# Kernel optimization log

Hardware: AMD Instinct MI355X
Metric: run time of the kernel (lower is better)

The kernel has to match this reference:

```python
import jax, jax.numpy as jnp
import numpy as np

GAMMA = 2.0                  # n2n_gamma
WAVELET_WEIGHT = 0.05
THRESHOLD = 50.0 / 255.0     # wavelet_threshold normalized
LEVELS = 3


def conv_model(x, weight):
    # Stand-in denoising network: 1->1 channel 3x3 SAME conv.
    return jax.lax.conv_general_dilated(
        x, weight, window_strides=(1, 1), padding='SAME',
        dimension_numbers=('NCHW', 'OIHW', 'NCHW'))


def generate_subimages_checkerboard(noisy):
    # 2x2 checkerboard: (even,even) and (odd,odd), bilinearly upsampled back
    # to (H, W). jax.image.resize 'linear' uses half-pixel centers, matching
    # torch F.interpolate(mode='bilinear', align_corners=False).
    B, C, H, W = noisy.shape  # H, W assumed even (512)
    p0 = noisy[:, :, 0::2, 0::2]
    p3 = noisy[:, :, 1::2, 1::2]
    g1 = jax.image.resize(p0, (B, C, H, W), method='linear')
    g2 = jax.image.resize(p3, (B, C, H, W), method='linear')
    return g1, g2


def haar_level(x):
    # One level of batched 2D Haar DWT on x: [B, H, W] (H, W even).
    a = x[:, 0::2, 0::2]
    b = x[:, 0::2, 1::2]
    c = x[:, 1::2, 0::2]
    d = x[:, 1::2, 1::2]
    ll = (a + b + c + d) * 0.5
    lh = (a - b + c - d) * 0.5  # horizontal detail
    hl = (a + b - c - d) * 0.5  # vertical detail
    hh = (a - b - c + d) * 0.5  # diagonal detail
    return ll, (lh, hl, hh)


def wavelet_sparsity_loss(pred):
    # pred: [B, C, H, W]; only channel 0 is used (as in the original).
    # L1(c, soft_threshold(c, t)) == mean(min(|c|, t)) since the target is
    # detached; pywt's coeffs[1] is the COARSEST detail level, with
    # threshold t/2^(level_idx-1) and weight 1/level_idx, so the finest
    # decomposition step j maps to level_idx = LEVELS - j + 1.
    x = pred[:, 0]  # [B, H, W]
    total = jnp.asarray(0.0, dtype=x.dtype)
    cur = x
    for j in range(1, LEVELS + 1):  # j=1 finest
        cur, (h, v, d) = haar_level(cur)
        level_idx = LEVELS - j + 1
        thr = THRESHOLD / (2.0 ** (level_idx - 1))
        w = 1.0 / level_idx
        lvl = (jnp.mean(jnp.minimum(jnp.abs(h), thr)) +
               jnp.mean(jnp.minimum(jnp.abs(v), thr)) +
               jnp.mean(jnp.minimum(jnp.abs(d), thr))) / 3.0
        total = total + w * lvl
    return total


def setup_inputs() -> dict:
    key = jax.random.key(0)
    k1, k2 = jax.random.split(key)
    noisy_input = jax.random.uniform(k1, (32, 1, 512, 512), dtype=jnp.float32)
    weight = jax.random.normal(k2, (1, 1, 3, 3), dtype=jnp.float32) * (1.0 / 3.0)
    return {"noisy_input": noisy_input, "weight": weight}


def reference(noisy_input, weight):
    g1, g2 = generate_subimages_checkerboard(noisy_input)
    out = jnp.clip(conv_model(g1, weight), 0.0, 1.0)
    rec = jnp.mean((out - g2) ** 2)
    reg = jnp.mean((out - g1) ** 2)
    n2n_total = rec + GAMMA * reg
    # Original detaches pred to numpy for the wavelet prior -> no gradient.
    wavelet = jax.lax.stop_gradient(wavelet_sparsity_loss(out))
    return n2n_total + WAVELET_WEIGHT * wavelet
```

## Files before the change

kernel.cpp:

```cpp
#include <hip/hip_runtime.h>

namespace {

constexpr int IMG = 512;
constexpr int S = 8;
constexpr int NSTRIPS = IMG / S;
constexpr int NWAVES = 32 * NSTRIPS;
constexpr int NBLK = NWAVES / 4;
constexpr float THR = 50.0f / 255.0f;

constexpr double N_PIX = 32.0 * 512.0 * 512.0;
constexpr double N_L1  = 32.0 * 256.0 * 256.0;
constexpr double N_L2  = 32.0 * 128.0 * 128.0;
constexpr double N_L3  = 32.0 * 64.0 * 64.0;
constexpr double C_REC = 1.0 / N_PIX;
constexpr double C_REG = 2.0 / N_PIX;
constexpr double C_W1  = 0.05 / (9.0 * N_L1);
constexpr double C_W2  = 0.05 / (6.0 * N_L2);
constexpr double C_W3  = 0.05 / (3.0 * N_L3);

struct F4 { float v[4]; };
struct F8 { float v[8]; };
struct Row { F8 g; float gl, gr; };

__device__ __forceinline__ F8 hblend(const F4& p, int lane) {
  float left  = __shfl_up(p.v[3], 1);
  float right = __shfl_down(p.v[0], 1);
  if (lane == 0)  left  = p.v[0];
  if (lane == 63) right = p.v[3];
  F8 h;
  h.v[0] = 0.25f*left   + 0.75f*p.v[0];
  h.v[1] = 0.75f*p.v[0] + 0.25f*p.v[1];
  h.v[2] = 0.25f*p.v[0] + 0.75f*p.v[1];
  h.v[3] = 0.75f*p.v[1] + 0.25f*p.v[2];
  h.v[4] = 0.25f*p.v[1] + 0.75f*p.v[2];
  h.v[5] = 0.75f*p.v[2] + 0.25f*p.v[3];
  h.v[6] = 0.25f*p.v[2] + 0.75f*p.v[3];
  h.v[7] = 0.75f*p.v[3] + 0.25f*right;
  return h;
}

__device__ __forceinline__ Row vblend(const F8& a, const F8& b, float wa, float wb, int lane) {
  Row r;
#pragma unroll
  for (int c = 0; c < 8; ++c) r.g.v[c] = wa*a.v[c] + wb*b.v[c];
  const float gl = __shfl_up(r.g.v[7], 1);
  const float gr = __shfl_down(r.g.v[0], 1);
  r.gl = (lane == 0)  ? 0.0f : gl;
  r.gr = (lane == 63) ? 0.0f : gr;
  return r;
}

__device__ __forceinline__ void conv_acc(const Row& r, const float* wk3, F8& acc) {
#pragma unroll
  for (int c = 0; c < 8; ++c) {
    const float gm1 = (c == 0) ? r.gl : r.g.v[c-1];
    const float gp1 = (c == 7) ? r.gr : r.g.v[c+1];
    acc.v[c] += wk3[0]*gm1 + wk3[1]*r.g.v[c] + wk3[2]*gp1;
  }
}

__device__ __forceinline__ F8 conv3(const Row& r0, const Row& r1, const Row& r2,
                                    const float* wk) {
  F8 o;
#pragma unroll
  for (int c = 0; c < 8; ++c) o.v[c] = 0.0f;
  conv_acc(r0, wk + 0, o);
  conv_acc(r1, wk + 3, o);
  conv_acc(r2, wk + 6, o);
#pragma unroll
  for (int c = 0; c < 8; ++c) o.v[c] = fminf(fmaxf(o.v[c], 0.0f), 1.0f);
  return o;
}

__device__ __forceinline__ F4 haarL1(const F8& e, const F8& o, float thr, float& acc) {
  F4 ll;
#pragma unroll
  for (int c = 0; c < 4; ++c) {
    const float a = e.v[2*c], b = e.v[2*c+1], cc = o.v[2*c], d = o.v[2*c+1];
    ll.v[c] = (a + b + cc + d) * 0.5f;
    const float lh = (a - b + cc - d) * 0.5f;
    const float hl = (a + b - cc - d) * 0.5f;
    const float hh = (a - b - cc + d) * 0.5f;
    acc += fminf(fabsf(lh), thr) + fminf(fabsf(hl), thr) + fminf(fabsf(hh), thr);
  }
  return ll;
}

__device__ __forceinline__ float haar1pair(float a, float b, float cc, float d,
                                           float thr, float& acc) {
  const float lh = (a - b + cc - d) * 0.5f;
  const float hl = (a + b - cc - d) * 0.5f;
  const float hh = (a - b - cc + d) * 0.5f;
  acc += fminf(fabsf(lh), thr) + fminf(fabsf(hl), thr) + fminf(fabsf(hh), thr);
  return (a + b + cc + d) * 0.5f;
}

__global__ __launch_bounds__(256, 2) void n2n_wavelet_kernel(
    const float* __restrict__ noisy,
    const float* __restrict__ weight,
    double* __restrict__ partial) {
  const int t = threadIdx.x;
  const int lane = t & 63;
  const int gwid = blockIdx.x * 4 + (t >> 6);
  const int strip = gwid & (NSTRIPS - 1);
  const int b = gwid >> 6;
  const float* base = noisy + (size_t)b * IMG * IMG + lane * 8;

  const int y0 = strip * S;
  const int k0 = y0 >> 1;
  const bool lastStrip = (y0 == IMG - S);

  float4 le0[6], le1[6], lo0[6], lo1[6];
#pragma unroll
  for (int i = 0; i < 6; ++i) {
    int r = k0 - 1 + i;
    r = r < 0 ? 0 : (r > 255 ? 255 : r);
    const float* pe = base + (2 * r) * IMG;
    const float* po = base + (2 * r + 1) * IMG;
    le0[i] = *(const float4*)pe;
    le1[i] = *(const float4*)(pe + 4);
    lo0[i] = *(const float4*)po;
    lo1[i] = *(const float4*)(po + 4);
  }

  float wk[9];
#pragma unroll
  for (int i = 0; i < 9; ++i) wk[i] = weight[i];

  F8 h0[6], h3[6];
#pragma unroll
  for (int i = 0; i < 6; ++i) {
    F4 e, o;
    e.v[0] = le0[i].x; e.v[1] = le0[i].z; e.v[2] = le1[i].x; e.v[3] = le1[i].z;
    o.v[0] = lo0[i].y; o.v[1] = lo0[i].w; o.v[2] = lo1[i].y; o.v[3] = lo1[i].w;
    h0[i] = hblend(e, lane);
    h3[i] = hblend(o, lane);
  }

  float rec = 0.f, rgg = 0.f, w1a = 0.f, w2a = 0.f, w3a = 0.f;
  const float thr1 = THR * 0.25f, thr2 = THR * 0.5f;

  Row g1m, g1c;
  if (y0 == 0) {
#pragma unroll
    for (int c = 0; c < 8; ++c) g1m.g.v[c] = 0.f;
    g1m.gl = 0.f; g1m.gr = 0.f;
  } else {
    g1m = vblend(h0[0], h0[1], 0.75f, 0.25f, lane);
  }
  g1c = vblend(h0[0], h0[1], 0.25f, 0.75f, lane);

  F4 ll1Prev;
  float ll2Prev0 = 0.f, ll2Prev1 = 0.f;

#pragma unroll
  for (int p = 0; p < 4; ++p) {
    const Row g1p = vblend(h0[p + 1], h0[p + 2], 0.75f, 0.25f, lane);

    const F8 outE = conv3(g1m, g1c, g1p, wk);
#pragma unroll
    for (int c = 0; c < 8; ++c) {
      const float g2 = 0.25f * h3[p].v[c] + 0.75f * h3[p + 1].v[c];
      float d = outE.v[c] - g2;        rec += d*d;
      d = outE.v[c] - g1c.g.v[c];      rgg += d*d;
    }

    Row g1q = vblend(h0[p + 1], h0[p + 2], 0.25f, 0.75f, lane);
    if (lastStrip && p == 3) {
#pragma unroll
      for (int c = 0; c < 8; ++c) g1q.g.v[c] = 0.f;
      g1q.gl = 0.f; g1q.gr = 0.f;
    }

    const F8 outO = conv3(g1c, g1p, g1q, wk);
#pragma unroll
    for (int c = 0; c < 8; ++c) {
      const float g2 = 0.75f * h3[p + 1].v[c] + 0.25f * h3[p + 2].v[c];
      float d = outO.v[c] - g2;        rec += d*d;
      d = outO.v[c] - g1p.g.v[c];      rgg += d*d;
    }

    const F4 ll1 = haarL1(outE, outO, thr1, w1a);
    if ((p & 1) == 0) {
      ll1Prev = ll1;
    } else {
      const float ll20 = haar1pair(ll1Prev.v[0], ll1Prev.v[1], ll1.v[0], ll1.v[1], thr2, w2a);
      const float ll21 = haar1pair(ll1Prev.v[2], ll1Prev.v[3], ll1.v[2], ll1.v[3], thr2, w2a);
      if (p == 1) {
        ll2Prev0 = ll20; ll2Prev1 = ll21;
      } else {
        const float lh = (ll2Prev0 - ll2Prev1 + ll20 - ll21) * 0.5f;
        const float hl = (ll2Prev0 + ll2Prev1 - ll20 - ll21) * 0.5f;
        const float hh = (ll2Prev0 - ll2Prev1 - ll20 + ll21) * 0.5f;
        w3a += fminf(fabsf(lh), THR) + fminf(fabsf(hl), THR) + fminf(fabsf(hh), THR);
      }
    }

    g1m = g1p; g1c = g1q;
  }

  float vals[5] = {rec, rgg, w1a, w2a, w3a};
#pragma unroll
  for (int v = 0; v < 5; ++v) {
#pragma unroll
    for (int off = 32; off > 0; off >>= 1) vals[v] += __shfl_down(vals[v], off);
  }
  if (lane == 0) {
    partial[gwid] = C_REC*(double)vals[0] + C_REG*(double)vals[1]
                  + C_W1*(double)vals[2] + C_W2*(double)vals[3] + C_W3*(double)vals[4];
  }
}

__global__ __launch_bounds__(256) void finalize_kernel(
    const double* __restrict__ partial, float* __restrict__ out) {
  __shared__ double sRed[4];
  const int t = threadIdx.x;
  double s = 0.0;
#pragma unroll
  for (int i = 0; i < NWAVES / 256; ++i) s += partial[i * 256 + t];
#pragma unroll
  for (int off = 32; off > 0; off >>= 1) s += __shfl_down(s, off);
  if ((t & 63) == 0) sRed[t >> 6] = s;
  __syncthreads();
  if (t == 0) out[0] = (float)(sRed[0] + sRed[1] + sRed[2] + sRed[3]);
}

}

extern "C" void kernel_launch(void* const* d_in, const int* in_sizes, int n_in,
                              void* d_out, int out_size, void* d_ws, size_t ws_size,
                              hipStream_t stream) {
  const float* noisy  = (const float*)d_in[0];
  const float* weight = (const float*)d_in[1];
  double* partial = (double*)d_ws;
  float* out = (float*)d_out;

  hipLaunchKernelGGL(n2n_wavelet_kernel, dim3(NBLK), dim3(256), 0, stream,
                     noisy, weight, partial);
  hipLaunchKernelGGL(finalize_kernel, dim3(1), dim3(256), 0, stream, partial, out);
}
```

Baseline: 84.39 us.

## Halve strip height and pair waves via shared memory for level-3 Haar

Each wave now handles 4 output rows instead of 8, and blocks shrink to two waves, which doubles the number of waves and cuts per-wave register use. Because a level-3 Haar coefficient spans 8 rows, the two waves in a block exchange level-2 LL values through shared memory with a barrier. The weights are also made wave-uniform with readfirstlane. The intent is more occupancy and latency hiding, at the cost of more redundant halo row loads and blending per output row, plus a block-level sync.

Measured after the change: 89.11 us. 5.6% more time.

```diff
diff --git a/kernel.cpp b/kernel.cpp
--- a/kernel.cpp
+++ b/kernel.cpp
@@ -3,10 +3,10 @@
 namespace {
 
 constexpr int IMG = 512;
-constexpr int S = 8;
+constexpr int S = 4;
 constexpr int NSTRIPS = IMG / S;
 constexpr int NWAVES = 32 * NSTRIPS;
-constexpr int NBLK = NWAVES / 4;
+constexpr int NBLK = NWAVES / 2;
 constexpr float THR = 50.0f / 255.0f;
 
 constexpr double N_PIX = 32.0 * 512.0 * 512.0;
@@ -96,44 +96,42 @@
   return (a + b + cc + d) * 0.5f;
 }
 
-__global__ __launch_bounds__(256, 2) void n2n_wavelet_kernel(
+__global__ __launch_bounds__(128, 3) void n2n_wavelet_kernel(
     const float* __restrict__ noisy,
     const float* __restrict__ weight,
     double* __restrict__ partial) {
+  __shared__ float ll2sh[128];
   const int t = threadIdx.x;
   const int lane = t & 63;
-  const int gwid = blockIdx.x * 4 + (t >> 6);
+  const int widx = t >> 6;
+  const int gwid = blockIdx.x * 2 + widx;
   const int strip = gwid & (NSTRIPS - 1);
-  const int b = gwid >> 6;
+  const int b = gwid >> 7;
   const float* base = noisy + (size_t)b * IMG * IMG + lane * 8;
 
   const int y0 = strip * S;
   const int k0 = y0 >> 1;
-  const bool lastStrip = (y0 == IMG - S);
-
-  float4 le0[6], le1[6], lo0[6], lo1[6];
-#pragma unroll
-  for (int i = 0; i < 6; ++i) {
+  const bool lastStrip = (strip == NSTRIPS - 1);
+
+  float wk[9];
+#pragma unroll
+  for (int i = 0; i < 9; ++i)
+    wk[i] = __uint_as_float(__builtin_amdgcn_readfirstlane(__float_as_uint(weight[i])));
+
+  F8 h0[4], h3[4];
+#pragma unroll
+  for (int i = 0; i < 4; ++i) {
     int r = k0 - 1 + i;
     r = r < 0 ? 0 : (r > 255 ? 255 : r);
-    const float* pe = base + (2 * r) * IMG;
-    const float* po = base + (2 * r + 1) * IMG;
-    le0[i] = *(const float4*)pe;
-    le1[i] = *(const float4*)(pe + 4);
-    lo0[i] = *(const float4*)po;
-    lo1[i] = *(const float4*)(po + 4);
-  }
-
-  float wk[9];
-#pragma unroll
-  for (int i = 0; i < 9; ++i) wk[i] = weight[i];
-
-  F8 h0[6], h3[6];
-#pragma unroll
-  for (int i = 0; i < 6; ++i) {
+    const float* pe = base + (size_t)(2 * r) * IMG;
+    const float* po = pe + IMG;
+    const float4 e0 = *(const float4*)pe;
+    const float4 e1 = *(const float4*)(pe + 4);
+    const float4 o0 = *(const float4*)po;
+    const float4 o1 = *(const float4*)(po + 4);
     F4 e, o;
-    e.v[0] = le0[i].x; e.v[1] = le0[i].z; e.v[2] = le1[i].x; e.v[3] = le1[i].z;
-    o.v[0] = lo0[i].y; o.v[1] = lo0[i].w; o.v[2] = lo1[i].y; o.v[3] = lo1[i].w;
+    e.v[0] = e0.x; e.v[1] = e0.z; e.v[2] = e1.x; e.v[3] = e1.z;
+    o.v[0] = o0.y; o.v[1] = o0.w; o.v[2] = o1.y; o.v[3] = o1.w;
     h0[i] = hblend(e, lane);
     h3[i] = hblend(o, lane);
   }
@@ -152,10 +150,10 @@
   g1c = vblend(h0[0], h0[1], 0.25f, 0.75f, lane);
 
   F4 ll1Prev;
-  float ll2Prev0 = 0.f, ll2Prev1 = 0.f;
-
-#pragma unroll
-  for (int p = 0; p < 4; ++p) {
+  float ll20 = 0.f, ll21 = 0.f;
+
+#pragma unroll
+  for (int p = 0; p < 2; ++p) {
     const Row g1p = vblend(h0[p + 1], h0[p + 2], 0.75f, 0.25f, lane);
 
     const F8 outE = conv3(g1m, g1c, g1p, wk);
@@ -167,7 +165,7 @@
     }
 
     Row g1q = vblend(h0[p + 1], h0[p + 2], 0.25f, 0.75f, lane);
-    if (lastStrip && p == 3) {
+    if (lastStrip && p == 1) {
 #pragma unroll
       for (int c = 0; c < 8; ++c) g1q.g.v[c] = 0.f;
       g1q.gl = 0.f; g1q.gr = 0.f;
@@ -182,22 +180,28 @@
     }
 
     const F4 ll1 = haarL1(outE, outO, thr1, w1a);
-    if ((p & 1) == 0) {
+    if (p == 0) {
       ll1Prev = ll1;
     } else {
-      const float ll20 = haar1pair(ll1Prev.v[0], ll1Prev.v[1], ll1.v[0], ll1.v[1], thr2, w2a);
-      const float ll21 = haar1pair(ll1Prev.v[2], ll1Prev.v[3], ll1.v[2], ll1.v[3], thr2, w2a);
-      if (p == 1) {
-        ll2Prev0 = ll20; ll2Prev1 = ll21;
-      } else {
-        const float lh = (ll2Prev0 - ll2Prev1 + ll20 - ll21) * 0.5f;
-        const float hl = (ll2Prev0 + ll2Prev1 - ll20 - ll21) * 0.5f;
-        const float hh = (ll2Prev0 - ll2Prev1 - ll20 + ll21) * 0.5f;
-        w3a += fminf(fabsf(lh), THR) + fminf(fabsf(hl), THR) + fminf(fabsf(hh), THR);
-      }
+      ll20 = haar1pair(ll1Prev.v[0], ll1Prev.v[1], ll1.v[0], ll1.v[1], thr2, w2a);
+      ll21 = haar1pair(ll1Prev.v[2], ll1Prev.v[3], ll1.v[2], ll1.v[3], thr2, w2a);
     }
 
     g1m = g1p; g1c = g1q;
+  }
+
+  if (widx == 0) {
+    ll2sh[2 * lane]     = ll20;
+    ll2sh[2 * lane + 1] = ll21;
+  }
+  __syncthreads();
+  if (widx == 1) {
+    const float a  = ll2sh[2 * lane];
+    const float bb = ll2sh[2 * lane + 1];
+    const float lh = (a - bb + ll20 - ll21) * 0.5f;
+    const float hl = (a + bb - ll20 - ll21) * 0.5f;
+    const float hh = (a - bb - ll20 + ll21) * 0.5f;
+    w3a += fminf(fabsf(lh), THR) + fminf(fabsf(hl), THR) + fminf(fabsf(hh), THR);
   }
 
   float vals[5] = {rec, rgg, w1a, w2a, w3a};
@@ -236,7 +240,7 @@
   double* partial = (double*)d_ws;
   float* out = (float*)d_out;
 
-  hipLaunchKernelGGL(n2n_wavelet_kernel, dim3(NBLK), dim3(256), 0, stream,
+  hipLaunchKernelGGL(n2n_wavelet_kernel, dim3(NBLK), dim3(128), 0, stream,
                      noisy, weight, partial);
   hipLaunchKernelGGL(finalize_kernel, dim3(1), dim3(256), 0, stream, partial, out);
 }
```

## Share halo source rows between waves via LDS instead of reloading from global

Applied to the files above, without the earlier changes.

Each wave now loads only its four own source row pairs from global memory. The halo row pairs above and below come from neighbouring waves in the same block, exchanged through shared memory with a block barrier. Only the first and last wave of a block still fetch their outer halos from global. The conv weights are made wave-uniform with readfirstlane. This trims redundant global loads and hblend work at the cost of LDS traffic and a __syncthreads. Correctness relies on the four waves of a block holding consecutive strips of the same image, which holds because there are 64 strips per image.

After: 83.80 us. No clear change (-0.7%).

```diff
diff --git a/kernel.cpp b/kernel.cpp
--- a/kernel.cpp
+++ b/kernel.cpp
@@ -40,6 +40,21 @@
   return h;
 }
 
+__device__ __forceinline__ void loadPair(const float* __restrict__ base, int r,
+                                         F8& h0o, F8& h3o, int lane) {
+  const float* pe = base + (size_t)(2 * r) * IMG;
+  const float* po = pe + IMG;
+  const float4 e0 = *(const float4*)pe;
+  const float4 e1 = *(const float4*)(pe + 4);
+  const float4 o0 = *(const float4*)po;
+  const float4 o1 = *(const float4*)(po + 4);
+  F4 e, o;
+  e.v[0] = e0.x; e.v[1] = e0.z; e.v[2] = e1.x; e.v[3] = e1.z;
+  o.v[0] = o0.y; o.v[1] = o0.w; o.v[2] = o1.y; o.v[3] = o1.w;
+  h0o = hblend(e, lane);
+  h3o = hblend(o, lane);
+}
+
 __device__ __forceinline__ Row vblend(const F8& a, const F8& b, float wa, float wb, int lane) {
   Row r;
 #pragma unroll
@@ -96,47 +111,65 @@
   return (a + b + cc + d) * 0.5f;
 }
 
+__device__ __forceinline__ void storeSh(float4 (&s)[2][2][64], const F8& a,
+                                        const F8& b, int lane) {
+  s[0][0][lane] = make_float4(a.v[0], a.v[1], a.v[2], a.v[3]);
+  s[0][1][lane] = make_float4(a.v[4], a.v[5], a.v[6], a.v[7]);
+  s[1][0][lane] = make_float4(b.v[0], b.v[1], b.v[2], b.v[3]);
+  s[1][1][lane] = make_float4(b.v[4], b.v[5], b.v[6], b.v[7]);
+}
+
+__device__ __forceinline__ void loadSh(const float4 (&s)[2][2][64], F8& a,
+                                       F8& b, int lane) {
+  const float4 a0 = s[0][0][lane], a1 = s[0][1][lane];
+  const float4 b0 = s[1][0][lane], b1 = s[1][1][lane];
+  a.v[0] = a0.x; a.v[1] = a0.y; a.v[2] = a0.z; a.v[3] = a0.w;
+  a.v[4] = a1.x; a.v[5] = a1.y; a.v[6] = a1.z; a.v[7] = a1.w;
+  b.v[0] = b0.x; b.v[1] = b0.y; b.v[2] = b0.z; b.v[3] = b0.w;
+  b.v[4] = b1.x; b.v[5] = b1.y; b.v[6] = b1.z; b.v[7] = b1.w;
+}
+
 __global__ __launch_bounds__(256, 2) void n2n_wavelet_kernel(
     const float* __restrict__ noisy,
     const float* __restrict__ weight,
     double* __restrict__ partial) {
+  __shared__ float4 sh[8][2][2][64];
   const int t = threadIdx.x;
   const int lane = t & 63;
-  const int gwid = blockIdx.x * 4 + (t >> 6);
+  const int widx = t >> 6;
+  const int gwid = blockIdx.x * 4 + widx;
   const int strip = gwid & (NSTRIPS - 1);
   const int b = gwid >> 6;
   const float* base = noisy + (size_t)b * IMG * IMG + lane * 8;
 
   const int y0 = strip * S;
   const int k0 = y0 >> 1;
-  const bool lastStrip = (y0 == IMG - S);
-
-  float4 le0[6], le1[6], lo0[6], lo1[6];
-#pragma unroll
-  for (int i = 0; i < 6; ++i) {
-    int r = k0 - 1 + i;
-    r = r < 0 ? 0 : (r > 255 ? 255 : r);
-    const float* pe = base + (2 * r) * IMG;
-    const float* po = base + (2 * r + 1) * IMG;
-    le0[i] = *(const float4*)pe;
-    le1[i] = *(const float4*)(pe + 4);
-    lo0[i] = *(const float4*)po;
-    lo1[i] = *(const float4*)(po + 4);
-  }
+  const bool lastStrip = (strip == NSTRIPS - 1);
 
   float wk[9];
 #pragma unroll
-  for (int i = 0; i < 9; ++i) wk[i] = weight[i];
+  for (int i = 0; i < 9; ++i)
+    wk[i] = __uint_as_float(__builtin_amdgcn_readfirstlane(__float_as_uint(weight[i])));
 
   F8 h0[6], h3[6];
 #pragma unroll
-  for (int i = 0; i < 6; ++i) {
-    F4 e, o;
-    e.v[0] = le0[i].x; e.v[1] = le0[i].z; e.v[2] = le1[i].x; e.v[3] = le1[i].z;
-    o.v[0] = lo0[i].y; o.v[1] = lo0[i].w; o.v[2] = lo1[i].y; o.v[3] = lo1[i].w;
-    h0[i] = hblend(e, lane);
-    h3[i] = hblend(o, lane);
-  }
+  for (int wi = 1; wi <= 4; ++wi)
+    loadPair(base, k0 + (wi - 1), h0[wi], h3[wi], lane);
+
+  if (widx == 0) {
+    int r = k0 - 1; r = r < 0 ? 0 : r;
+    loadPair(base, r, h0[0], h3[0], lane);
+  }
+  if (widx == 3) {
+    int r = k0 + 4; r = r > 255 ? 255 : r;
+    loadPair(base, r, h0[5], h3[5], lane);
+  }
+
+  storeSh(sh[2 * widx],     h0[1], h3[1], lane);
+  storeSh(sh[2 * widx + 1], h0[4], h3[4], lane);
+  __syncthreads();
+  if (widx > 0) loadSh(sh[2 * widx - 1], h0[0], h3[0], lane);
+  if (widx < 3) loadSh(sh[2 * widx + 2], h0[5], h3[5], lane);
 
   float rec = 0.f, rgg = 0.f, w1a = 0.f, w2a = 0.f, w3a = 0.f;
   const float thr1 = THR * 0.25f, thr2 = THR * 0.5f;
```
